# Kernel tuning notes

Measured on AMD Instinct MI355X. Metric: run time of the kernel, lower is better.

The kernel has to match this reference:

```python
import jax, jax.numpy as jnp
import numpy as np


def _dht(x):
    # Hartley transform via full fftn over ALL dims (matches torch dht2d(x, dim=None))
    f = jnp.fft.fftn(x)
    return f.real + f.imag


def setup_inputs() -> dict:
    key = jax.random.key(0)
    ks = jax.random.split(key, 5)
    B, H, W, C = 2, 128, 256, 768
    nb, fac = 8, 1
    bs = C // nb
    scale = 0.02
    x = jax.random.normal(ks[0], (B, H, W, C), dtype=jnp.float32)
    w1 = scale * jax.random.normal(ks[1], (2, nb, bs, bs * fac), dtype=jnp.float32)
    b1 = scale * jax.random.normal(ks[2], (2, nb, bs * fac), dtype=jnp.float32)
    w2 = scale * jax.random.normal(ks[3], (2, nb, bs * fac, bs), dtype=jnp.float32)
    b2 = scale * jax.random.normal(ks[4], (2, nb, bs), dtype=jnp.float32)
    return {"x": x, "w1": w1, "b1": b1, "w2": w2, "b2": b2}


def reference(x, w1, b1, w2, b2):
    SPARSITY = 0.01
    FRAC = 1.0  # hard_thresholding_fraction
    bias = x
    B, H, W, C = x.shape
    nb = w1.shape[1]
    bs = C // nb
    xf = x.astype(jnp.float32)

    X_k = _dht(xf).reshape(B, H, W, nb, bs)
    X_nk = jnp.roll(jnp.flip(xf, axis=(1, 2)), shift=(1, 1), axis=(1, 2)).reshape(B, H, W, nb, bs)

    total = H // 2 + 1
    kept = int(total * FRAC)
    r0, r1 = total - kept, min(total + kept, H)  # row slice clamps like torch slicing

    a = X_k[:, r0:r1, :kept]    # [B, Hs, kept, nb, bs]
    an = X_nk[:, r0:r1, :kept]

    ein = lambda t, w: jnp.einsum('bhwni,nio->bhwno', t, w)

    o1_k = jax.nn.relu(0.5 * (ein(a, w1[0]) - ein(an, w1[1]) + ein(a, w1[1]) + ein(an, w1[0])) + b1[0])
    o1_nk = jax.nn.relu(0.5 * (ein(an, w1[0]) - ein(a, w1[1]) + ein(an, w1[1]) + ein(a, w1[0])) + b1[1])

    o2_k = 0.5 * (ein(o1_k, w2[0]) - ein(o1_nk, w2[1]) + ein(o1_k, w2[1]) + ein(o1_nk, w2[0])) + b2[0]
    # NOTE: source genuinely uses o2_k (not o1_k) in two terms here; kept faithful.
    o2_nk = 0.5 * (ein(o1_nk, w2[0]) - ein(o2_k, w2[1]) + ein(o1_nk, w2[1]) + ein(o2_k, w2[0])) + b2[1]

    s = o2_k + o2_nk
    # softshrink
    s = jnp.sign(s) * jnp.maximum(jnp.abs(s) - SPARSITY, 0.0)

    full = jnp.zeros((B, H, W, nb, bs), jnp.float32).at[:, r0:r1, :kept].set(s)
    full = full.reshape(B, H, W, C)
    out = _dht(full) / full.size  # idht2d with dim=None: normalize by numel
    return out.astype(x.dtype) + bias
```

## Files before the change

### kernel.cpp

```cpp
#include <hip/hip_runtime.h>

#define BB 2
#define HH 128
#define WW 256
#define CC 768
#define NB 8
#define BS 96
#define WKEPT 65
#define NPTS (BB*HH*WKEPT)
#define NTOT ((size_t)BB*HH*WW*CC)
#define TWOPI 6.283185307179586f

typedef __attribute__((ext_vector_type(8))) short bf16x8;
typedef __attribute__((ext_vector_type(4))) float f32x4;

__device__ __forceinline__ unsigned short f2bf(float f) {
    unsigned int u = __float_as_uint(f);
    u += 0x7fffu + ((u >> 16) & 1u);
    return (unsigned short)(u >> 16);
}
__device__ __forceinline__ float bf2f(unsigned short s) {
    return __uint_as_float((unsigned int)s << 16);
}

__global__ __launch_bounds__(256) void k_weights(
    const float* __restrict__ w1, const float* __restrict__ w2,
    const float* __restrict__ b2,
    unsigned short* __restrict__ W10h, unsigned short* __restrict__ W10l,
    unsigned short* __restrict__ W11h, unsigned short* __restrict__ W11l,
    unsigned short* __restrict__ WKPh, unsigned short* __restrict__ WKPl,
    unsigned short* __restrict__ WKMh, unsigned short* __restrict__ WKMl,
    float* __restrict__ BEFF)
{
    const int n = blockIdx.x;
    const int tid = threadIdx.x;
    __shared__ float m_s[BS*BS];

    const float* w2a = w2 + (size_t)(0*NB + n)*BS*BS;
    const float* w2b = w2 + (size_t)(1*NB + n)*BS*BS;
    for (int idx = tid; idx < BS*BS; idx += 256)
        m_s[idx] = 0.5f*(w2a[idx] - w2b[idx]);

    const float* w1a = w1 + (size_t)(0*NB + n)*BS*BS;
    const float* w1b = w1 + (size_t)(1*NB + n)*BS*BS;
    for (int idx = tid; idx < BS*BS; idx += 256) {
        int o = idx / BS, k = idx - o*BS;
        float v0 = w1a[k*BS + o];
        unsigned short h0 = f2bf(v0);
        unsigned short l0 = f2bf(v0 - bf2f(h0));
        W10h[n*BS*BS + idx] = h0;  W10l[n*BS*BS + idx] = l0;
        float v1 = w1b[k*BS + o];
        unsigned short h1 = f2bf(v1);
        unsigned short l1 = f2bf(v1 - bf2f(h1));
        W11h[n*BS*BS + idx] = h1;  W11l[n*BS*BS + idx] = l1;
    }
    __syncthreads();

    for (int idx = tid; idx < BS*BS; idx += 256) {
        int i = idx / BS, o = idx - i*BS;
        float p_io = 0.5f*(w2a[idx] + w2b[idx]);
        float m_io = m_s[idx];
        float accK = 0.f, accN = 0.f;
        for (int j = 0; j < BS; ++j) {
            float p_ij = 0.5f*(w2a[i*BS + j] + w2b[i*BS + j]);
            float mjo  = m_s[j*BS + o];
            accK += p_ij * mjo;
            accN += m_s[i*BS + j] * mjo;
        }
        float valK = p_io + accK;
        float valN = p_io + m_io + accN;
        float wkp = 0.5f*(valK + valN);
        float wkm = 0.5f*(valK - valN);
        int d = n*BS*BS + o*BS + i;
        unsigned short hp = f2bf(wkp);
        WKPh[d] = hp;  WKPl[d] = f2bf(wkp - bf2f(hp));
        unsigned short hm = f2bf(wkm);
        WKMh[d] = hm;  WKMl[d] = f2bf(wkm - bf2f(hm));
    }
    if (tid < BS) {
        const float* b2a = b2 + (0*NB + n)*BS;
        const float* b2b = b2 + (1*NB + n)*BS;
        float acc = b2a[tid] + b2b[tid];
        for (int j = 0; j < BS; ++j) acc += b2a[j] * m_s[j*BS + tid];
        BEFF[n*BS + tid] = acc;
    }
}

__global__ __launch_bounds__(256) void k_p1(
    const float* __restrict__ x, float2* __restrict__ out)
{
    const int tid = threadIdx.x;
    const int row = blockIdx.y;
    const int c0 = blockIdx.x * 16;
    __shared__ float2 tw[256];
    __shared__ float2 bufA[8*256];
    __shared__ float2 bufB[8*256];

    {
        float sn, cs; sincosf(TWOPI*(float)tid/256.f, &sn, &cs);
        tw[tid] = make_float2(cs, -sn);
    }
    const float* xr = x + (size_t)row * WW * CC + c0;
    for (int idx = tid; idx < 2048; idx += 256) {
        int l = idx & 7, w = idx >> 3;
        const float2 v = *(const float2*)(xr + (size_t)w*CC + 2*l);
        bufA[l*256 + w] = v;
    }
    __syncthreads();

    float2* src = bufA;
    float2* dst = bufB;
    const int t  = tid & 127;
    const int l0 = tid >> 7;
    #pragma unroll
    for (int st = 0; st < 8; ++st) {
        const int s = 1 << st;
        const int q = t & (s - 1);
        const int p = t >> st;
        const float2 w = tw[p << st];
        #pragma unroll
        for (int k = 0; k < 4; ++k) {
            int base = (l0 + 2*k) * 256;
            float2 a = src[base + q + s*p];
            float2 b = src[base + q + s*p + 128];
            float dx = a.x - b.x, dy = a.y - b.y;
            dst[base + q + 2*s*p]     = make_float2(a.x + b.x, a.y + b.y);
            dst[base + q + 2*s*p + s] = make_float2(dx*w.x - dy*w.y, dx*w.y + dy*w.x);
        }
        __syncthreads();
        float2* tmp = src; src = dst; dst = tmp;
    }
    for (int idx = tid; idx < 8*WKEPT; idx += 256) {
        int l = idx & 7, wp = idx >> 3;
        float2 Z  = src[l*256 + wp];
        float2 Zm = src[l*256 + ((256 - wp) & 255)];
        float2 U = make_float2(0.5f*(Z.x + Zm.x), 0.5f*(Z.y - Zm.y));
        float2 V = make_float2(0.5f*(Z.y + Zm.y), 0.5f*(Zm.x - Z.x));
        size_t g = (size_t)(row*WKEPT + wp)*CC + c0 + 2*l;
        out[g]     = U;
        out[g + 1] = V;
    }
}

#define LPB 4
__global__ __launch_bounds__(256) void k_cfft(
    const float2* __restrict__ in, float2* __restrict__ out)
{
    __shared__ float2 tw[CC];
    __shared__ float2 bufA[LPB*CC];
    __shared__ float2 bufB[LPB*CC];
    const int tid = threadIdx.x;
    const size_t line0 = (size_t)blockIdx.x * LPB;

    for (int t = tid; t < CC; t += 256) {
        float sn, cs; sincosf(TWOPI * (float)t / 768.0f, &sn, &cs);
        tw[t] = make_float2(cs, -sn);
    }
    for (int idx = tid; idx < LPB*CC; idx += 256) {
        int l = idx / CC, c = idx - l*CC;
        int m = c / 3, j = c - 3*m;
        bufA[l*CC + j*256 + m] = in[(line0 + l)*CC + c];
    }
    __syncthreads();

    float2* src = bufA;
    float2* dst = bufB;
    #pragma unroll
    for (int st = 0; st < 8; ++st) {
        const int s = 1 << st;
        const int h = 128 >> st;
        for (int item = tid; item < LPB*3*128; item += 256) {
            int sub = item >> 7;
            int t   = item & 127;
            int q = t & (s - 1);
            int p = t >> st;
            float2 a = src[sub*256 + q + s*p];
            float2 b = src[sub*256 + q + s*(p + h)];
            float2 w = tw[p * (3 << st)];
            float dx = a.x - b.x, dy = a.y - b.y;
            dst[sub*256 + q + s*(2*p)]     = make_float2(a.x + b.x, a.y + b.y);
            dst[sub*256 + q + s*(2*p + 1)] = make_float2(dx*w.x - dy*w.y, dx*w.y + dy*w.x);
        }
        __syncthreads();
        float2* tmp = src; src = dst; dst = tmp;
    }
    for (int idx = tid; idx < LPB*CC; idx += 256) {
        int l = idx / CC, cp = idx - l*CC;
        int r = cp & 255;
        float2 S0 = src[(l*3 + 0)*256 + r];
        float2 S1 = src[(l*3 + 1)*256 + r];
        float2 S2 = src[(l*3 + 2)*256 + r];
        float2 w1 = tw[cp];
        int i2 = 2*cp; if (i2 >= CC) i2 -= CC;
        float2 w2 = tw[i2];
        float fr = S0.x + w1.x*S1.x - w1.y*S1.y + w2.x*S2.x - w2.y*S2.y;
        float fi = S0.y + w1.x*S1.y + w1.y*S1.x + w2.x*S2.y + w2.y*S2.x;
        out[(line0 + l)*CC + cp] = make_float2(fr, fi);
    }
}

__global__ __launch_bounds__(256) void k_hb_c2a(
    const float2* __restrict__ in, float* __restrict__ aout)
{
    const int tid = threadIdx.x;
    const int wp = blockIdx.y;
    const int c0 = blockIdx.x * 8;
    __shared__ float2 tw[128];
    __shared__ float2 bufA[16*128];
    __shared__ float2 bufB[16*128];

    if (tid < 128) {
        float sn, cs; sincosf(TWOPI*(float)tid/128.f, &sn, &cs);
        tw[tid] = make_float2(cs, -sn);
    }
    for (int idx = tid; idx < 1024; idx += 256) {
        int cl = idx & 7, h = idx >> 3;
        float2 z0 = in[(size_t)((0*HH + h)*WKEPT + wp)*CC + c0 + cl];
        float2 z1 = in[(size_t)((1*HH + h)*WKEPT + wp)*CC + c0 + cl];
        bufA[(2*cl+0)*128 + h] = make_float2(z0.x+z1.x, z0.y+z1.y);
        bufA[(2*cl+1)*128 + h] = make_float2(z0.x-z1.x, z0.y-z1.y);
    }
    __syncthreads();

    float2* src = bufA;
    float2* dst = bufB;
    const int t  = tid & 63;
    const int l0 = tid >> 6;
    #pragma unroll
    for (int st = 0; st < 7; ++st) {
        const int s = 1 << st;
        const int q = t & (s - 1);
        const int p = t >> st;
        const float2 w = tw[p << st];
        #pragma unroll
        for (int k = 0; k < 4; ++k) {
            int base = (l0 + 4*k) * 128;
            float2 a = src[base + q + s*p];
            float2 b = src[base + q + s*p + 64];
            float dx = a.x - b.x, dy = a.y - b.y;
            dst[base + q + 2*s*p]     = make_float2(a.x + b.x, a.y + b.y);
            dst[base + q + 2*s*p + s] = make_float2(dx*w.x - dy*w.y, dx*w.y + dy*w.x);
        }
        __syncthreads();
        float2* tmp = src; src = dst; dst = tmp;
    }
    for (int idx = tid; idx < 2048; idx += 256) {
        int cl = idx & 7;
        int hp = (idx >> 3) & 127;
        int uv = idx >> 10;
        float2 z = src[(2*cl + uv)*128 + hp];
        aout[(size_t)((uv*HH + hp)*WKEPT + wp)*CC + c0 + cl] = z.x + z.y;
    }
}

__global__ __launch_bounds__(256) void k_hb_s2c(
    const float* __restrict__ sreal, float2* __restrict__ out)
{
    const int tid = threadIdx.x;
    const int wp = blockIdx.y;
    const int c0 = blockIdx.x * 16;
    __shared__ float2 tw[128];
    __shared__ float2 bufA[16*128];
    __shared__ float2 bufB[16*128];

    if (tid < 128) {
        float sn, cs; sincosf(TWOPI*(float)tid/128.f, &sn, &cs);
        tw[tid] = make_float2(cs, -sn);
    }
    for (int idx = tid; idx < 2048; idx += 256) {
        int cl = idx & 15, h = idx >> 4;
        float s0 = sreal[(size_t)((0*HH + h)*WKEPT + wp)*CC + c0 + cl];
        float s1 = sreal[(size_t)((1*HH + h)*WKEPT + wp)*CC + c0 + cl];
        bufA[cl*128 + h] = make_float2(s0 + s1, s0 - s1);
    }
    __syncthreads();

    float2* src = bufA;
    float2* dst = bufB;
    const int t  = tid & 63;
    const int l0 = tid >> 6;
    #pragma unroll
    for (int st = 0; st < 7; ++st) {
        const int s = 1 << st;
        const int q = t & (s - 1);
        const int p = t >> st;
        const float2 w = tw[p << st];
        #pragma unroll
        for (int k = 0; k < 4; ++k) {
            int base = (l0 + 4*k) * 128;
            float2 a = src[base + q + s*p];
            float2 b = src[base + q + s*p + 64];
            float dx = a.x - b.x, dy = a.y - b.y;
            dst[base + q + 2*s*p]     = make_float2(a.x + b.x, a.y + b.y);
            dst[base + q + 2*s*p + s] = make_float2(dx*w.x - dy*w.y, dx*w.y + dy*w.x);
        }
        __syncthreads();
        float2* tmp = src; src = dst; dst = tmp;
    }
    for (int idx = tid; idx < 2048; idx += 256) {
        int cl = idx & 15;
        int hp = idx >> 4;
        float2 A  = src[cl*128 + hp];
        float2 Zm = src[cl*128 + ((128 - hp) & 127)];
        float2 U = make_float2(0.5f*(A.x + Zm.x), 0.5f*(A.y - Zm.y));
        float2 V = make_float2(0.5f*(A.y + Zm.y), 0.5f*(Zm.x - A.x));
        out[(size_t)((0*HH + hp)*WKEPT + wp)*CC + c0 + cl] = U;
        out[(size_t)((1*HH + hp)*WKEPT + wp)*CC + c0 + cl] = V;
    }
}

__global__ __launch_bounds__(256, 2) void k_mlp(
    const float* __restrict__ a, const float* __restrict__ x,
    const unsigned short* __restrict__ W10h, const unsigned short* __restrict__ W10l,
    const unsigned short* __restrict__ W11h, const unsigned short* __restrict__ W11l,
    const unsigned short* __restrict__ WKPh, const unsigned short* __restrict__ WKPl,
    const unsigned short* __restrict__ WKMh, const unsigned short* __restrict__ WKMl,
    const float* __restrict__ b1, const float* __restrict__ BEFF,
    float* __restrict__ sout)
{
    const int tid = threadIdx.x;
    const int n = blockIdx.y;
    const int P0 = blockIdx.x * 64;
    __shared__ unsigned short Wh_A[96*48], Wl_A[96*48];
    __shared__ unsigned short Wh_B[96*48], Wl_B[96*48];
    __shared__ unsigned short PMp[64*104], PMm[64*104];

    const int lane = tid & 63;
    const int wv = tid >> 6;
    const int lr = lane & 15;
    const int lk = lane >> 4;

    const int Pld = P0 + 16*wv + lr;
    int bb = Pld / (HH*WKEPT);
    int rem = Pld - bb*(HH*WKEPT);
    int h = rem / WKEPT;
    int wq = rem - h*WKEPT;
    int hh2 = (HH - h) & (HH-1);
    int ww2 = (WW - wq) & (WW-1);
    const float* aRow  = a + (size_t)Pld*CC + n*BS;
    const float* anRow = x + (size_t)((bb*HH + hh2)*WW + ww2)*CC + n*BS;

    f32x4 T1[6], T2[6];
    #pragma unroll
    for (int t = 0; t < 6; ++t) {
        T1[t] = (f32x4){0.f,0.f,0.f,0.f};
        T2[t] = (f32x4){0.f,0.f,0.f,0.f};
    }

    for (int ks = 0; ks < 3; ++ks) {
        __syncthreads();
        for (int idx = tid; idx < 96*16; idx += 256) {
            int o = idx >> 4, kp = (idx & 15) << 1;
            int g = n*BS*BS + o*BS + ks*32 + kp;
            *(ushort2*)&Wh_A[o*48 + kp] = *(const ushort2*)&W10h[g];
            *(ushort2*)&Wl_A[o*48 + kp] = *(const ushort2*)&W10l[g];
            *(ushort2*)&Wh_B[o*48 + kp] = *(const ushort2*)&W11h[g];
            *(ushort2*)&Wl_B[o*48 + kp] = *(const ushort2*)&W11l[g];
        }
        __syncthreads();

        const int kseg = ks*32 + 8*lk;
        float4 a0 = *(const float4*)(aRow + kseg);
        float4 a1 = *(const float4*)(aRow + kseg + 4);
        float4 n0 = *(const float4*)(anRow + kseg);
        float4 n1 = *(const float4*)(anRow + kseg + 4);
        bf16x8 uF, vF;
        uF[0] = (short)f2bf(0.5f*(a0.x + n0.x));  vF[0] = (short)f2bf(0.5f*(a0.x - n0.x));
        uF[1] = (short)f2bf(0.5f*(a0.y + n0.y));  vF[1] = (short)f2bf(0.5f*(a0.y - n0.y));
        uF[2] = (short)f2bf(0.5f*(a0.z + n0.z));  vF[2] = (short)f2bf(0.5f*(a0.z - n0.z));
        uF[3] = (short)f2bf(0.5f*(a0.w + n0.w));  vF[3] = (short)f2bf(0.5f*(a0.w - n0.w));
        uF[4] = (short)f2bf(0.5f*(a1.x + n1.x));  vF[4] = (short)f2bf(0.5f*(a1.x - n1.x));
        uF[5] = (short)f2bf(0.5f*(a1.y + n1.y));  vF[5] = (short)f2bf(0.5f*(a1.y - n1.y));
        uF[6] = (short)f2bf(0.5f*(a1.z + n1.z));  vF[6] = (short)f2bf(0.5f*(a1.z - n1.z));
        uF[7] = (short)f2bf(0.5f*(a1.w + n1.w));  vF[7] = (short)f2bf(0.5f*(a1.w - n1.w));

        #pragma unroll
        for (int t = 0; t < 6; ++t) {
            int wb = (16*t + lr)*48 + 8*lk;
            bf16x8 bh = *(const bf16x8*)&Wh_A[wb];
            T1[t] = __builtin_amdgcn_mfma_f32_16x16x32_bf16(uF, bh, T1[t], 0, 0, 0);
            bf16x8 bl = *(const bf16x8*)&Wl_A[wb];
            T1[t] = __builtin_amdgcn_mfma_f32_16x16x32_bf16(uF, bl, T1[t], 0, 0, 0);
            bf16x8 ch = *(const bf16x8*)&Wh_B[wb];
            T2[t] = __builtin_amdgcn_mfma_f32_16x16x32_bf16(vF, ch, T2[t], 0, 0, 0);
            bf16x8 cl = *(const bf16x8*)&Wl_B[wb];
            T2[t] = __builtin_amdgcn_mfma_f32_16x16x32_bf16(vF, cl, T2[t], 0, 0, 0);
        }
    }

    #pragma unroll
    for (int t = 0; t < 6; ++t) {
        float bk = b1[(0*NB + n)*BS + 16*t + lr];
        float bn = b1[(1*NB + n)*BS + 16*t + lr];
        #pragma unroll
        for (int r = 0; r < 4; ++r) {
            float ok = fmaxf(T1[t][r] + T2[t][r] + bk, 0.f);
            float on = fmaxf(T1[t][r] - T2[t][r] + bn, 0.f);
            int pl = 16*wv + 4*lk + r;
            PMp[pl*104 + 16*t + lr] = f2bf(ok + on);
            PMm[pl*104 + 16*t + lr] = f2bf(ok - on);
        }
    }

    f32x4 S[6];
    #pragma unroll
    for (int t = 0; t < 6; ++t) S[t] = (f32x4){0.f,0.f,0.f,0.f};
    for (int ks = 0; ks < 3; ++ks) {
        __syncthreads();
        for (int idx = tid; idx < 96*16; idx += 256) {
            int o = idx >> 4, kp = (idx & 15) << 1;
            int g = n*BS*BS + o*BS + ks*32 + kp;
            *(ushort2*)&Wh_A[o*48 + kp] = *(const ushort2*)&WKPh[g];
            *(ushort2*)&Wl_A[o*48 + kp] = *(const ushort2*)&WKPl[g];
            *(ushort2*)&Wh_B[o*48 + kp] = *(const ushort2*)&WKMh[g];
            *(ushort2*)&Wl_B[o*48 + kp] = *(const ushort2*)&WKMl[g];
        }
        __syncthreads();

        const int kseg = ks*32 + 8*lk;
        bf16x8 pF = *(const bf16x8*)&PMp[(16*wv + lr)*104 + kseg];
        bf16x8 mF = *(const bf16x8*)&PMm[(16*wv + lr)*104 + kseg];
        #pragma unroll
        for (int t = 0; t < 6; ++t) {
            int wb = (16*t + lr)*48 + 8*lk;
            bf16x8 bh = *(const bf16x8*)&Wh_A[wb];
            S[t] = __builtin_amdgcn_mfma_f32_16x16x32_bf16(pF, bh, S[t], 0, 0, 0);
            bf16x8 bl = *(const bf16x8*)&Wl_A[wb];
            S[t] = __builtin_amdgcn_mfma_f32_16x16x32_bf16(pF, bl, S[t], 0, 0, 0);
            bf16x8 ch = *(const bf16x8*)&Wh_B[wb];
            S[t] = __builtin_amdgcn_mfma_f32_16x16x32_bf16(mF, ch, S[t], 0, 0, 0);
            bf16x8 cl = *(const bf16x8*)&Wl_B[wb];
            S[t] = __builtin_amdgcn_mfma_f32_16x16x32_bf16(mF, cl, S[t], 0, 0, 0);
        }
    }

    #pragma unroll
    for (int t = 0; t < 6; ++t) {
        float be = BEFF[n*BS + 16*t + lr];
        #pragma unroll
        for (int r = 0; r < 4; ++r) {
            float v = S[t][r] + be;
            float av2 = fabsf(v) - 0.01f;
            float sv = (av2 > 0.f) ? copysignf(av2, v) : 0.f;
            int pt = P0 + 16*wv + 4*lk + r;
            sout[(size_t)pt*CC + n*BS + 16*t + lr] = sv;
        }
    }
}

__global__ __launch_bounds__(256) void k_p7(
    const float2* __restrict__ A, const float* __restrict__ x,
    float* __restrict__ out)
{
    const int tid = threadIdx.x;
    const int row = blockIdx.y;
    const int c0 = blockIdx.x * 8;
    __shared__ float2 tw[256];
    __shared__ float2 bufA[8*256];
    __shared__ float2 bufB[8*256];

    {
        float sn, cs; sincosf(TWOPI*(float)tid/256.f, &sn, &cs);
        tw[tid] = make_float2(cs, -sn);
    }
    const float2* Ar = A + (size_t)row * WKEPT * CC + c0;
    for (int idx = tid; idx < 2048; idx += 256) {
        int l = idx & 7, w = idx >> 3;
        bufA[l*256 + w] = (w < WKEPT) ? Ar[(size_t)w*CC + l]
                                      : make_float2(0.f, 0.f);
    }
    __syncthreads();

    float2* src = bufA;
    float2* dst = bufB;
    const int t  = tid & 127;
    const int l0 = tid >> 7;
    #pragma unroll
    for (int st = 0; st < 8; ++st) {
        const int s = 1 << st;
        const int q = t & (s - 1);
        const int p = t >> st;
        const float2 w = tw[p << st];
        #pragma unroll
        for (int k = 0; k < 4; ++k) {
            int base = (l0 + 2*k) * 256;
            float2 a = src[base + q + s*p];
            float2 b = src[base + q + s*p + 128];
            float dx = a.x - b.x, dy = a.y - b.y;
            dst[base + q + 2*s*p]     = make_float2(a.x + b.x, a.y + b.y);
            dst[base + q + 2*s*p + s] = make_float2(dx*w.x - dy*w.y, dx*w.y + dy*w.x);
        }
        __syncthreads();
        float2* tmp = src; src = dst; dst = tmp;
    }
    const float scale = 1.0f / 50331648.0f;
    const size_t obase = (size_t)row * WW * CC + c0;
    for (int idx = tid; idx < 2048; idx += 256) {
        int l = idx & 7, w = idx >> 3;
        float2 z = src[l*256 + w];
        size_t g = obase + (size_t)w*CC + l;
        out[g] = fmaf(z.x + z.y, scale, x[g]);
    }
}

extern "C" void kernel_launch(void* const* d_in, const int* in_sizes, int n_in,
                              void* d_out, int out_size, void* d_ws, size_t ws_size,
                              hipStream_t stream)
{
    (void)in_sizes; (void)n_in; (void)out_size; (void)ws_size;
    const float* x  = (const float*)d_in[0];
    const float* w1 = (const float*)d_in[1];
    const float* b1 = (const float*)d_in[2];
    const float* w2 = (const float*)d_in[3];
    const float* b2 = (const float*)d_in[4];

    float*  ws     = (float*)d_ws;
    float2* Abuf   = (float2*)d_ws;
    float*  a_real = ws;
    float*  s_real = ws + (size_t)NPTS*CC;
    float*  BEFF   = ws + 2*(size_t)NPTS*CC;
    unsigned short* Wq = (unsigned short*)(BEFF + NB*BS);
    const size_t WSZ = (size_t)NB*BS*BS;
    unsigned short* W10h = Wq + 0*WSZ;
    unsigned short* W10l = Wq + 1*WSZ;
    unsigned short* W11h = Wq + 2*WSZ;
    unsigned short* W11l = Wq + 3*WSZ;
    unsigned short* WKPh = Wq + 4*WSZ;
    unsigned short* WKPl = Wq + 5*WSZ;
    unsigned short* WKMh = Wq + 6*WSZ;
    unsigned short* WKMl = Wq + 7*WSZ;

    float2* Bc   = (float2*)d_out;
    float*  outf = (float*)d_out;

    k_weights<<<dim3(NB), dim3(256), 0, stream>>>(
        w1, w2, b2, W10h, W10l, W11h, W11l, WKPh, WKPl, WKMh, WKMl, BEFF);
    k_p1     <<<dim3(48, 256), dim3(256), 0, stream>>>(x, Abuf);
    k_cfft   <<<dim3(NPTS/LPB), dim3(256), 0, stream>>>(Abuf, Bc);
    k_hb_c2a <<<dim3(96, WKEPT), dim3(256), 0, stream>>>(Bc, a_real);
    k_mlp    <<<dim3(260, NB), dim3(256), 0, stream>>>(
        a_real, x, W10h, W10l, W11h, W11l, WKPh, WKPl, WKMh, WKMl,
        b1, BEFF, s_real);
    k_hb_s2c <<<dim3(48, WKEPT), dim3(256), 0, stream>>>(s_real, Bc);
    k_cfft   <<<dim3(NPTS/LPB), dim3(256), 0, stream>>>(Bc, Abuf);
    k_p7     <<<dim3(96, 256), dim3(256), 0, stream>>>(Abuf, x, outf);
}
```

Before: 1.146 ms.

## Rewrite final W-axis FFT as in-place DIF with 16 channels per block

The last-stage kernel now processes 16 channels per block instead of 8, halving the grid. Its Stockham FFT with two ping-pong buffers becomes an in-place decimation-in-frequency FFT in one padded shared buffer (stride 257), and bit-reversal is applied at output. The wider channel tile gives 64-byte contiguous global segments per row instead of 32, which should improve coalescing of loads and stores. In exchange it adds a register staging step and an extra barrier per stage, and the bit-reversed reads at output may cost some LDS efficiency.

```diff
diff --git a/kernel.cpp b/kernel.cpp
--- a/kernel.cpp
+++ b/kernel.cpp
@@ -454,51 +454,57 @@
 {
     const int tid = threadIdx.x;
     const int row = blockIdx.y;
-    const int c0 = blockIdx.x * 8;
-    __shared__ float2 tw[256];
-    __shared__ float2 bufA[8*256];
-    __shared__ float2 bufB[8*256];
-
-    {
+    const int c0 = blockIdx.x * 16;
+    __shared__ float2 tw[128];
+    __shared__ float2 buf[16*257];
+
+    if (tid < 128) {
         float sn, cs; sincosf(TWOPI*(float)tid/256.f, &sn, &cs);
         tw[tid] = make_float2(cs, -sn);
     }
     const float2* Ar = A + (size_t)row * WKEPT * CC + c0;
-    for (int idx = tid; idx < 2048; idx += 256) {
-        int l = idx & 7, w = idx >> 3;
-        bufA[l*256 + w] = (w < WKEPT) ? Ar[(size_t)w*CC + l]
-                                      : make_float2(0.f, 0.f);
+    for (int idx = tid; idx < 16*256; idx += 256) {
+        int l = idx & 15, w = idx >> 4;
+        buf[l*257 + w] = (w < WKEPT) ? Ar[(size_t)w*CC + l]
+                                     : make_float2(0.f, 0.f);
     }
     __syncthreads();
 
-    float2* src = bufA;
-    float2* dst = bufB;
-    const int t  = tid & 127;
-    const int l0 = tid >> 7;
+    const int l  = tid & 15;
+    const int tg = tid >> 4;
     #pragma unroll
     for (int st = 0; st < 8; ++st) {
-        const int s = 1 << st;
-        const int q = t & (s - 1);
-        const int p = t >> st;
-        const float2 w = tw[p << st];
-        #pragma unroll
-        for (int k = 0; k < 4; ++k) {
-            int base = (l0 + 2*k) * 256;
-            float2 a = src[base + q + s*p];
-            float2 b = src[base + q + s*p + 128];
+        const int h = 128 >> st;
+        float2 av[8], bv[8];
+        #pragma unroll
+        for (int k = 0; k < 8; ++k) {
+            int t = tg + 16*k;
+            int j = t & (h - 1);
+            int i = ((t >> (7 - st)) << (8 - st)) | j;
+            av[k] = buf[l*257 + i];
+            bv[k] = buf[l*257 + i + h];
+        }
+        __syncthreads();
+        #pragma unroll
+        for (int k = 0; k < 8; ++k) {
+            int t = tg + 16*k;
+            int j = t & (h - 1);
+            int i = ((t >> (7 - st)) << (8 - st)) | j;
+            float2 w = tw[j << st];
+            float2 a = av[k], b = bv[k];
             float dx = a.x - b.x, dy = a.y - b.y;
-            dst[base + q + 2*s*p]     = make_float2(a.x + b.x, a.y + b.y);
-            dst[base + q + 2*s*p + s] = make_float2(dx*w.x - dy*w.y, dx*w.y + dy*w.x);
-        }
-        __syncthreads();
-        float2* tmp = src; src = dst; dst = tmp;
+            buf[l*257 + i]     = make_float2(a.x + b.x, a.y + b.y);
+            buf[l*257 + i + h] = make_float2(dx*w.x - dy*w.y, dx*w.y + dy*w.x);
+        }
+        __syncthreads();
     }
     const float scale = 1.0f / 50331648.0f;
     const size_t obase = (size_t)row * WW * CC + c0;
-    for (int idx = tid; idx < 2048; idx += 256) {
-        int l = idx & 7, w = idx >> 3;
-        float2 z = src[l*256 + w];
-        size_t g = obase + (size_t)w*CC + l;
+    for (int idx = tid; idx < 16*256; idx += 256) {
+        int l2 = idx & 15, w = idx >> 4;
+        int rb = (int)(__brev((unsigned)w) >> 24);
+        float2 z = buf[l2*257 + rb];
+        size_t g = obase + (size_t)w*CC + l2;
         out[g] = fmaf(z.x + z.y, scale, x[g]);
     }
 }
@@ -543,5 +549,5 @@
         b1, BEFF, s_real);
     k_hb_s2c <<<dim3(48, WKEPT), dim3(256), 0, stream>>>(s_real, Bc);
     k_cfft   <<<dim3(NPTS/LPB), dim3(256), 0, stream>>>(Bc, Abuf);
-    k_p7     <<<dim3(96, 256), dim3(256), 0, stream>>>(Abuf, x, outf);
-}
+    k_p7     <<<dim3(48, 256), dim3(256), 0, stream>>>(Abuf, x, outf);
+}
```

After: 1.023 ms. 10.7% less time.
